# Kernel tuning notes

Measured on AMD Instinct MI355X. Metric: run time of the kernel, lower is better.

The kernel has to match this reference:

```python
import jax, jax.numpy as jnp
import numpy as np
import math

B, S, D = 2, 4096, 1024
H, HD = 16, 64
R = 16

def _rope(x, cos, sin):
    # x: [B, S, H, HD]; cos/sin: [S, HD//2]
    xr = x.reshape(*x.shape[:-1], HD // 2, 2)
    xe, xo = xr[..., 0], xr[..., 1]
    c = cos[None, :, None, :]
    s = sin[None, :, None, :]
    # complex multiply (xe + i*xo) * (c + i*s)
    re = xe * c - xo * s
    im = xe * s + xo * c
    return jnp.stack([re, im], axis=-1).reshape(x.shape)

def setup_inputs() -> dict:
    key = jax.random.key(0)
    ks = jax.random.split(key, 20)
    inp = {}
    inp["x"] = jax.random.normal(ks[0], (B, S, D), dtype=jnp.float32)
    pos = jnp.arange(S, dtype=jnp.float32)
    inv_freq = 1.0 / (10000.0 ** (jnp.arange(0, HD, 2, dtype=jnp.float32) / HD))
    ang = pos[:, None] * inv_freq[None, :]  # [S, HD//2]
    inp["freqs_cos"] = jnp.cos(ang)
    inp["freqs_sin"] = jnp.sin(ang)
    causal = jnp.triu(jnp.full((S, S), -1e9, dtype=jnp.float32), k=1)
    inp["mask"] = causal[None, None, :, :]
    sc = 1.0 / math.sqrt(D)
    inp["wq_w"] = jax.random.normal(ks[1], (D, D), dtype=jnp.float32) * sc
    inp["wq_b"] = jnp.zeros((D,), dtype=jnp.float32)
    inp["wk_w"] = jax.random.normal(ks[2], (D, D), dtype=jnp.float32) * sc
    inp["wv_w"] = jax.random.normal(ks[3], (D, D), dtype=jnp.float32) * sc
    inp["wo_w"] = jax.random.normal(ks[4], (D, D), dtype=jnp.float32) * sc
    inp["wo_b"] = jnp.zeros((D,), dtype=jnp.float32)
    for i, nm in enumerate(["q", "k", "v", "o"]):
        inp[f"lora_{nm}_l1"] = jax.random.normal(ks[5 + 2 * i], (R, D), dtype=jnp.float32) * sc
        inp[f"lora_{nm}_l2"] = jax.random.normal(ks[6 + 2 * i], (D, R), dtype=jnp.float32) * 0.01
    return inp

def reference(x, freqs_cos, freqs_sin, mask, wq_w, wq_b, wk_w, wv_w, wo_w, wo_b,
              lora_q_l1, lora_q_l2, lora_k_l1, lora_k_l2,
              lora_v_l1, lora_v_l2, lora_o_l1, lora_o_l2):
    # QKV projections + LoRA deltas (torch Linear: y = x @ W.T + b, W is [out, in])
    xq = x @ wq_w.T + wq_b + (x @ lora_q_l1.T) @ lora_q_l2.T
    xk = x @ wk_w.T + (x @ lora_k_l1.T) @ lora_k_l2.T
    xv = x @ wv_w.T + (x @ lora_v_l1.T) @ lora_v_l2.T
    xq = xq.reshape(B, S, H, HD)
    xk = xk.reshape(B, S, H, HD)
    xv = xv.reshape(B, S, H, HD)
    xq = _rope(xq, freqs_cos, freqs_sin)
    xk = _rope(xk, freqs_cos, freqs_sin)
    # attention (training path: keys/values = current xk/xv, causal mask additive)
    scores = jnp.einsum('bqhd,bkhd->bhqk', xq, xk) / math.sqrt(HD)
    scores = scores + mask
    probs = jax.nn.softmax(scores.astype(jnp.float32), axis=-1).astype(xq.dtype)
    out = jnp.einsum('bhqk,bkhd->bqhd', probs, xv).reshape(B, S, D)
    return out @ wo_w.T + wo_b + (out @ lora_o_l1.T) @ lora_o_l2.T
```

## Files before the change

### kernel.cpp

```cpp
#include <hip/hip_runtime.h>
#include <hip/hip_bf16.h>
#include <stdint.h>

#define S_DIM 4096
#define D_DIM 1024
#define KAUG  1088
#define M_ROWS 8192

typedef short bf16x8 __attribute__((ext_vector_type(8)));
typedef float f32x4  __attribute__((ext_vector_type(4)));

__device__ __forceinline__ f32x4 mfma16(bf16x8 a, bf16x8 b, f32x4 c) {
  return __builtin_amdgcn_mfma_f32_16x16x32_bf16(a, b, c, 0, 0, 0);
}
__device__ __forceinline__ short f2bs(float f) {
  __hip_bfloat16 h = __float2bfloat16(f);
  return *reinterpret_cast<short*>(&h);
}
__device__ __forceinline__ short f2bs_fast(float f) {
  unsigned u = __builtin_bit_cast(unsigned, f) + 0x8000u;
  return (short)(u >> 16);
}
__device__ __forceinline__ unsigned pk2bf(float a, float b) {
  unsigned ua = __builtin_bit_cast(unsigned, a) + 0x8000u;
  unsigned ub = __builtin_bit_cast(unsigned, b) + 0x8000u;
  return __builtin_amdgcn_perm(ub, ua, 0x07060302);
}
__device__ __forceinline__ float bs2f(short s) {
  __hip_bfloat16 h;
  *reinterpret_cast<short*>(&h) = s;
  return __bfloat162float(h);
}
__device__ __forceinline__ float fexp2(float x) {
  return __builtin_amdgcn_exp2f(x);
}
__device__ __forceinline__ void gload16(const void* g, void* l) {
  __builtin_amdgcn_global_load_lds(
      (const __attribute__((address_space(1))) unsigned int*)g,
      (__attribute__((address_space(3))) unsigned int*)l, 16, 0, 0);
}

__global__ void prep_k(const float* __restrict__ x,
                       const float* __restrict__ wq, const float* __restrict__ wk,
                       const float* __restrict__ wv, const float* __restrict__ wo,
                       const float* __restrict__ wqb,
                       const float* __restrict__ lq1, const float* __restrict__ lq2,
                       const float* __restrict__ lk1, const float* __restrict__ lk2,
                       const float* __restrict__ lv1, const float* __restrict__ lv2,
                       const float* __restrict__ lo1, const float* __restrict__ lo2,
                       const float* __restrict__ cf, const float* __restrict__ sf,
                       short* __restrict__ xaug, short* __restrict__ wqkv,
                       short* __restrict__ woaug, short* __restrict__ l1cat,
                       float* __restrict__ biasc, float* __restrict__ cs2)
{
  unsigned i = blockIdx.x * 256u + threadIdx.x;
  if (i < 8388608u) {
    unsigned m = i >> 10, k = i & 1023u;
    xaug[(size_t)m * KAUG + k] = f2bs(x[i]);
    return;
  }
  i -= 8388608u;
  if (i < 3342336u) {
    unsigned n = i / 1088u, k = i - n * 1088u;
    float v;
    if (k < 1024u) {
      v = (n < 1024u) ? wq[n * 1024u + k]
        : (n < 2048u) ? wk[(n - 1024u) * 1024u + k]
                      : wv[(n - 2048u) * 1024u + k];
    } else {
      unsigned r = k - 1024u, blk = r >> 4, which = n >> 10;
      if (blk == which) {
        const float* l2 = which == 0 ? lq2 : which == 1 ? lk2 : lv2;
        v = l2[(n & 1023u) * 16u + (r & 15u)];
      } else v = 0.f;
    }
    wqkv[i] = f2bs(v);
    return;
  }
  i -= 3342336u;
  if (i < 1114112u) {
    unsigned n = i / 1088u, k = i - n * 1088u;
    float v = (k < 1024u) ? wo[n * 1024u + k]
            : (k < 1040u) ? lo2[n * 16u + (k - 1024u)] : 0.f;
    woaug[i] = f2bs(v);
    return;
  }
  i -= 1114112u;
  if (i < 65536u) {
    unsigned r = i >> 10, k = i & 1023u;
    const float* src = r < 16u ? lq1 : r < 32u ? lk1 : r < 48u ? lv1 : lo1;
    l1cat[i] = f2bs(src[(r & 15u) * 1024u + k]);
    return;
  }
  i -= 65536u;
  if (i < 3072u) {
    biasc[i] = (i < 1024u) ? wqb[i] : 0.f;
    return;
  }
  i -= 3072u;
  if (i < 131072u) {
    cs2[2u * i]     = cf[i];
    cs2[2u * i + 1] = sf[i];
  }
}

template<int MODE>
__global__ __launch_bounds__(256) void gemm_bt(
    const short* __restrict__ A, int lda,
    const short* __restrict__ B, int ldb,
    int N, int K,
    const float* __restrict__ bias,
    void* __restrict__ Cout, int ldc, int colofs,
    short* __restrict__ qo, short* __restrict__ ko, short* __restrict__ vo,
    const float* __restrict__ cs2)
{
  __shared__ short As[128 * 32];
  __shared__ short Bs[128 * 32];
  const int tid = threadIdx.x;
  const int w = tid >> 6, lane = tid & 63;
  const int q4 = lane >> 4, c = lane & 15;
  const int mh = w >> 1, nh = w & 1;
  const int mt = blockIdx.y, nt = blockIdx.x;

  const int rl = lane >> 2;
  const int kc = (lane & 3) * 8;

  const short* Ag0 = A + (size_t)(mt * 128 + w * 32 + rl) * lda + kc;
  const short* Ag1 = Ag0 + (size_t)16 * lda;
  int rb0 = nt * 128 + w * 32 + rl;      if (rb0 > N - 1) rb0 = N - 1;
  int rb1 = nt * 128 + w * 32 + 16 + rl; if (rb1 > N - 1) rb1 = N - 1;
  const short* Bg0 = B + (size_t)rb0 * ldb + kc;
  const short* Bg1 = B + (size_t)rb1 * ldb + kc;
  short* as0 = &As[(w * 32) * 32];
  short* as1 = &As[(w * 32 + 16) * 32];
  short* bs0 = &Bs[(w * 32) * 32];
  short* bs1 = &Bs[(w * 32 + 16) * 32];

  f32x4 acc[4][4];
#pragma unroll
  for (int ms = 0; ms < 4; ++ms)
#pragma unroll
    for (int ns = 0; ns < 4; ++ns) acc[ms][ns] = (f32x4){0.f, 0.f, 0.f, 0.f};

  const int nkt = K >> 5;
  for (int kt = 0; kt < nkt; ++kt) {
    __syncthreads();
    gload16(Ag0, as0);
    gload16(Ag1, as1);
    gload16(Bg0, bs0);
    gload16(Bg1, bs1);
    Ag0 += 32; Ag1 += 32; Bg0 += 32; Bg1 += 32;
    __syncthreads();
    bf16x8 af[4], bfr[4];
#pragma unroll
    for (int ms = 0; ms < 4; ++ms)
      af[ms] = *(const bf16x8*)&As[(mh * 64 + ms * 16 + c) * 32 + q4 * 8];
#pragma unroll
    for (int ns = 0; ns < 4; ++ns)
      bfr[ns] = *(const bf16x8*)&Bs[(nh * 64 + ns * 16 + c) * 32 + q4 * 8];
#pragma unroll
    for (int ms = 0; ms < 4; ++ms)
#pragma unroll
      for (int ns = 0; ns < 4; ++ns)
        acc[ms][ns] = mfma16(af[ms], bfr[ns], acc[ms][ns]);
  }

#pragma unroll
  for (int ms = 0; ms < 4; ++ms) {
#pragma unroll
    for (int ns = 0; ns < 4; ++ns) {
      const int n = nt * 128 + nh * 64 + ns * 16 + c;
      if (MODE == 0) {
        float bsv = (n < N) ? bias[n] : 0.f;
        float* Co = (float*)Cout;
#pragma unroll
        for (int r = 0; r < 4; ++r) {
          int m = mt * 128 + mh * 64 + ms * 16 + q4 * 4 + r;
          if (n < N) Co[(size_t)m * ldc + n] = acc[ms][ns][r] + bsv;
        }
      } else if (MODE == 1) {
        short* Co = (short*)Cout;
#pragma unroll
        for (int r = 0; r < 4; ++r) {
          int m = mt * 128 + mh * 64 + ms * 16 + q4 * 4 + r;
          if (n < N) Co[(size_t)m * ldc + colofs + n] = f2bs_fast(acc[ms][ns][r]);
        }
      } else {
        float bsv = bias[n];
        int which = n >> 10;
        int m0 = mt * 128 + mh * 64 + ms * 16 + q4 * 4;
        int bb = m0 >> 12, spos = m0 & 4095;
        if (which < 2) {
          int h = (n >> 6) & 15;
          int hd = n & 63;
          short* dst = which == 0 ? qo : ko;
          const float sgn = (c & 1) ? 1.f : -1.f;
          const int ihalf = hd >> 1;
#pragma unroll
          for (int r = 0; r < 4; ++r) {
            float val = acc[ms][ns][r] + bsv;
            float part = __shfl_xor(val, 1);
            float2 cs = *(const float2*)&cs2[((size_t)(spos + r) * 32 + ihalf) * 2];
            float res = val * cs.x + part * (sgn * cs.y);
            if (which == 0) res *= 0.18033688011112042f;
            dst[(size_t)((bb * 16 + h) * 4096 + spos + r) * 64 + hd] = f2bs_fast(res);
          }
        } else {
          int h = (n >> 6) & 15;
          int hd = n & 63;
          uint2 vk;
          vk.x = pk2bf(acc[ms][ns][0] + bsv, acc[ms][ns][1] + bsv);
          vk.y = pk2bf(acc[ms][ns][2] + bsv, acc[ms][ns][3] + bsv);
          *(uint2*)&vo[(((size_t)bb * 16 + h) * 64 + hd) * 4096 + spos] = vk;
        }
      }
    }
  }
}

template<int NT>
__global__ __launch_bounds__(256) void tgemm_k(
    const short* __restrict__ A, int lda,
    const short* __restrict__ B, int ldb,
    int N, int K, short* __restrict__ C, int ldc, int colofs)
{
  __shared__ short As[64 * 32];
  __shared__ short Bs[64 * 32];
  const int tid = threadIdx.x;
  const int w = tid >> 6, lane = tid & 63;
  const int q4 = lane >> 4, c = lane & 15;
  const int rl = lane >> 2, kc = (lane & 3) * 8;
  const int arow = w * 16 + rl;
  const int brow = arow <= N - 1 ? arow : N - 1;

  const short* Ag = A + (size_t)(blockIdx.x * 64 + arow) * lda + kc;
  const short* Bg = B + (size_t)brow * ldb + kc;
  short* asd = &As[(w * 16) * 32];
  short* bsd = &Bs[(w * 16) * 32];

  f32x4 acc[NT];
#pragma unroll
  for (int i = 0; i < NT; ++i) acc[i] = (f32x4){0.f, 0.f, 0.f, 0.f};

  const int nkt = K >> 5;
  for (int kt = 0; kt < nkt; ++kt) {
    __syncthreads();
    gload16(Ag, asd);
    gload16(Bg, bsd);
    Ag += 32; Bg += 32;
    __syncthreads();
    bf16x8 af = *(const bf16x8*)&As[(w * 16 + c) * 32 + q4 * 8];
#pragma unroll
    for (int nsi = 0; nsi < NT; ++nsi) {
      bf16x8 bf = *(const bf16x8*)&Bs[(nsi * 16 + c) * 32 + q4 * 8];
      acc[nsi] = mfma16(af, bf, acc[nsi]);
    }
  }
#pragma unroll
  for (int nsi = 0; nsi < NT; ++nsi) {
#pragma unroll
    for (int r = 0; r < 4; ++r) {
      int m = blockIdx.x * 64 + w * 16 + q4 * 4 + r;
      int n = nsi * 16 + c;
      if (n < N) C[(size_t)m * ldc + colofs + n] = f2bs_fast(acc[nsi][r]);
    }
  }
}

__global__ __launch_bounds__(256, 2) void flash_k(
    const short* __restrict__ Qb, const short* __restrict__ Kb,
    const short* __restrict__ Vt, short* __restrict__ Oaug)
{
  __shared__ short lds[24576];
  short* const PL = &lds[16384];

  const int id = (int)blockIdx.y * 16 + (int)blockIdx.x;
  const int g = id & 7, j = id >> 3;
  const int bh = g * 4 + (j >> 4);
  const int bx = j & 15;

  const int tid = threadIdx.x;
  const int w = tid >> 6, lane = tid & 63;
  const int q4 = lane >> 4, c = lane & 15;

  const short* Kg = Kb + (size_t)bh * 4096 * 64;
  const short* Vg = Vt + (size_t)bh * 64 * 4096;

  const int l8 = lane >> 3, l7 = lane & 7;
  const int sw = (l7 ^ l8) * 8;
  const int G0 = w * 2, G1 = w * 2 + 1;
  const int koff0 = (G0 * 8 + l8) * 64 + sw;
  const int koff1 = (G1 * 8 + l8) * 64 + sw;
  const int voff0 = (G0 * 8 + l8) * 4096 + sw;
  const int voff1 = (G1 * 8 + l8) * 4096 + sw;
  const int qg = w * 4;
  const int qoff0 = ((qg + 0) * 8 + l8) * 64 + sw;
  const int qoff1 = ((qg + 1) * 8 + l8) * 64 + sw;
  const int qoff2 = ((qg + 2) * 8 + l8) * 64 + sw;
  const int qoff3 = ((qg + 3) * 8 + l8) * 64 + sw;

  const int c7 = c & 7;
  const int chA0 = ((q4) ^ c7) * 8;
  const int chA1 = ((4 + q4) ^ c7) * 8;
  const int rowc = c * 64;
  const int rowq = (w * 16 + c) * 64;
  const int pw_base = (w * 16 + c) * 64 + (q4 & 1) * 4;
  const int pw_g = q4 >> 1;

  const int b = bh >> 4, h = bh & 15;

  for (int half = 0; half < 2; ++half) {
    const int qt = half == 0 ? 31 - bx : bx;
    const short* Qg = Qb + ((size_t)bh * 4096 + qt * 128) * 64;

    gload16(Qg + qoff0, &lds[16384 + (qg + 0) * 512]);
    gload16(Qg + qoff1, &lds[16384 + (qg + 1) * 512]);
    gload16(Qg + qoff2, &lds[16384 + (qg + 2) * 512]);
    gload16(Qg + qoff3, &lds[16384 + (qg + 3) * 512]);
    gload16(Kg + koff0, &lds[G0 * 512]);
    gload16(Kg + koff1, &lds[G1 * 512]);
    gload16(Vg + voff0, &lds[8192 + G0 * 512]);
    gload16(Vg + voff1, &lds[8192 + G1 * 512]);
    __syncthreads();

    bf16x8 qa0 = *(const bf16x8*)(PL + rowq + chA0);
    bf16x8 qa1 = *(const bf16x8*)(PL + rowq + chA1);
    bf16x8 qb0 = *(const bf16x8*)(PL + 4096 + rowq + chA0);
    bf16x8 qb1 = *(const bf16x8*)(PL + 4096 + rowq + chA1);

    f32x4 oa[4], ob[4];
#pragma unroll
    for (int i = 0; i < 4; ++i) {
      oa[i] = (f32x4){0.f, 0.f, 0.f, 0.f};
      ob[i] = (f32x4){0.f, 0.f, 0.f, 0.f};
    }
    float la = 0.f, lb = 0.f;

    const int last = 2 * qt + 1;
    for (int kt = 0; kt <= last; ++kt) {
      const int cur = (kt & 1) * 4096;
      const short* Kc = &lds[cur];
      const short* Vc = &lds[8192 + cur];
      if (kt < last) {
        const int nxt = ((kt + 1) & 1) * 4096;
        const short* ks = Kg + (size_t)(kt + 1) * 4096;
        const short* vs = Vg + (size_t)(kt + 1) * 64;
        gload16(ks + koff0, &lds[nxt + G0 * 512]);
        gload16(ks + koff1, &lds[nxt + G1 * 512]);
        gload16(vs + voff0, &lds[8192 + nxt + G0 * 512]);
        gload16(vs + voff1, &lds[8192 + nxt + G1 * 512]);
      }
      const bool doA = (kt <= 2 * qt);

      f32x4 sa[4], sb[4];
#pragma unroll
      for (int ns = 0; ns < 4; ++ns) {
        bf16x8 kf0 = *(const bf16x8*)(Kc + ns * 1024 + rowc + chA0);
        bf16x8 kf1 = *(const bf16x8*)(Kc + ns * 1024 + rowc + chA1);
        sa[ns] = mfma16(kf0, qa0, (f32x4){0.f, 0.f, 0.f, 0.f});
        sa[ns] = mfma16(kf1, qa1, sa[ns]);
        sb[ns] = mfma16(kf0, qb0, (f32x4){0.f, 0.f, 0.f, 0.f});
        sb[ns] = mfma16(kf1, qb1, sb[ns]);
      }
      if (kt == 2 * qt) {
#pragma unroll
        for (int ns = 0; ns < 4; ++ns)
#pragma unroll
          for (int r = 0; r < 4; ++r)
            if (ns * 16 + q4 * 4 + r > w * 16 + c) sa[ns][r] = -1e30f;
      }
      if (kt == last) {
#pragma unroll
        for (int ns = 0; ns < 4; ++ns)
#pragma unroll
          for (int r = 0; r < 4; ++r)
            if (ns * 16 + q4 * 4 + r > w * 16 + c) sb[ns][r] = -1e30f;
      }

      bf16x8 pfa0, pfa1;
      if (doA) {
        float ps[4][4];
#pragma unroll
        for (int ns = 0; ns < 4; ++ns)
#pragma unroll
          for (int r = 0; r < 4; ++r) ps[ns][r] = fexp2(sa[ns][r]);
        float s0 = (ps[0][0] + ps[0][1]) + (ps[0][2] + ps[0][3]);
        float s1 = (ps[1][0] + ps[1][1]) + (ps[1][2] + ps[1][3]);
        float s2 = (ps[2][0] + ps[2][1]) + (ps[2][2] + ps[2][3]);
        float s3 = (ps[3][0] + ps[3][1]) + (ps[3][2] + ps[3][3]);
        float sum = (s0 + s1) + (s2 + s3);
        sum += __shfl_xor(sum, 16);
        sum += __shfl_xor(sum, 32);
        la += sum;
#pragma unroll
        for (int ns = 0; ns < 4; ++ns) {
          uint2 pk;
          pk.x = pk2bf(ps[ns][0], ps[ns][1]);
          pk.y = pk2bf(ps[ns][2], ps[ns][3]);
          *(uint2*)(PL + pw_base + (((ns * 2 + pw_g) ^ c7) * 8)) = pk;
        }
        pfa0 = *(const bf16x8*)(PL + rowq + chA0);
        pfa1 = *(const bf16x8*)(PL + rowq + chA1);
      }
      {
        float ps[4][4];
#pragma unroll
        for (int ns = 0; ns < 4; ++ns)
#pragma unroll
          for (int r = 0; r < 4; ++r) ps[ns][r] = fexp2(sb[ns][r]);
        float s0 = (ps[0][0] + ps[0][1]) + (ps[0][2] + ps[0][3]);
        float s1 = (ps[1][0] + ps[1][1]) + (ps[1][2] + ps[1][3]);
        float s2 = (ps[2][0] + ps[2][1]) + (ps[2][2] + ps[2][3]);
        float s3 = (ps[3][0] + ps[3][1]) + (ps[3][2] + ps[3][3]);
        float sum = (s0 + s1) + (s2 + s3);
        sum += __shfl_xor(sum, 16);
        sum += __shfl_xor(sum, 32);
        lb += sum;
#pragma unroll
        for (int ns = 0; ns < 4; ++ns) {
          uint2 pk;
          pk.x = pk2bf(ps[ns][0], ps[ns][1]);
          pk.y = pk2bf(ps[ns][2], ps[ns][3]);
          *(uint2*)(PL + 4096 + pw_base + (((ns * 2 + pw_g) ^ c7) * 8)) = pk;
        }
      }
      bf16x8 pfb0 = *(const bf16x8*)(PL + 4096 + rowq + chA0);
      bf16x8 pfb1 = *(const bf16x8*)(PL + 4096 + rowq + chA1);

#pragma unroll
      for (int nc = 0; nc < 4; ++nc) {
        bf16x8 vf0 = *(const bf16x8*)(Vc + nc * 1024 + rowc + chA0);
        bf16x8 vf1 = *(const bf16x8*)(Vc + nc * 1024 + rowc + chA1);
        if (doA) {
          oa[nc] = mfma16(vf0, pfa0, oa[nc]);
          oa[nc] = mfma16(vf1, pfa1, oa[nc]);
        }
        ob[nc] = mfma16(vf0, pfb0, ob[nc]);
        ob[nc] = mfma16(vf1, pfb1, ob[nc]);
      }
      __syncthreads();
    }

    float lia = 1.f / la, lib = 1.f / lb;
#pragma unroll
    for (int nc = 0; nc < 4; ++nc) {
      uint2 ok;
      ok.x = pk2bf(oa[nc][0] * lia, oa[nc][1] * lia);
      ok.y = pk2bf(oa[nc][2] * lia, oa[nc][3] * lia);
      *(uint2*)(PL + pw_base + (((nc * 2 + pw_g) ^ c7) * 8)) = ok;
      uint2 ok2;
      ok2.x = pk2bf(ob[nc][0] * lib, ob[nc][1] * lib);
      ok2.y = pk2bf(ob[nc][2] * lib, ob[nc][3] * lib);
      *(uint2*)(PL + 4096 + pw_base + (((nc * 2 + pw_g) ^ c7) * 8)) = ok2;
    }
    __syncthreads();
#pragma unroll
    for (int i2 = 0; i2 < 4; ++i2) {
      int ch = tid + i2 * 256;
      int r = ch >> 3, g2 = ch & 7;
      size_t row = (size_t)b * 4096 + qt * 128 + r;
      *(int4*)&Oaug[row * KAUG + h * 64 + g2 * 8] =
          *(const int4*)(PL + r * 64 + ((g2 ^ (r & 7)) * 8));
    }
    __syncthreads();
  }
}

extern "C" void kernel_launch(void* const* d_in, const int* in_sizes, int n_in,
                              void* d_out, int out_size, void* d_ws, size_t ws_size,
                              hipStream_t stream) {
  const float* x   = (const float*)d_in[0];
  const float* fc  = (const float*)d_in[1];
  const float* fs  = (const float*)d_in[2];
  const float* wq  = (const float*)d_in[4];
  const float* wqb = (const float*)d_in[5];
  const float* wk  = (const float*)d_in[6];
  const float* wv  = (const float*)d_in[7];
  const float* wo  = (const float*)d_in[8];
  const float* wob = (const float*)d_in[9];
  const float* lq1 = (const float*)d_in[10];
  const float* lq2 = (const float*)d_in[11];
  const float* lk1 = (const float*)d_in[12];
  const float* lk2 = (const float*)d_in[13];
  const float* lv1 = (const float*)d_in[14];
  const float* lv2 = (const float*)d_in[15];
  const float* lo1 = (const float*)d_in[16];
  const float* lo2 = (const float*)d_in[17];

  char* ws = (char*)d_ws;
  const size_t OFF_XAUG  = 0;
  const size_t OFF_XOAUG = 17825792;
  const size_t OFF_WQKV  = 35651584;
  const size_t OFF_WOAUG = 42336256;
  const size_t OFF_L1CAT = 44564480;
  const size_t OFF_BIASC = 44695552;
  const size_t OFF_QB    = 44707840;
  const size_t OFF_KB    = 61485056;
  const size_t OFF_VT    = 78262272;
  const size_t OFF_CS    = 95039488;

  short* xaug  = (short*)(ws + OFF_XAUG);
  short* xoaug = (short*)(ws + OFF_XOAUG);
  short* wqkv  = (short*)(ws + OFF_WQKV);
  short* woaug = (short*)(ws + OFF_WOAUG);
  short* l1cat = (short*)(ws + OFF_L1CAT);
  float* biasc = (float*)(ws + OFF_BIASC);
  short* qb    = (short*)(ws + OFF_QB);
  short* kb    = (short*)(ws + OFF_KB);
  short* vt    = (short*)(ws + OFF_VT);
  float* cs2   = (float*)(ws + OFF_CS);

  prep_k<<<50956, 256, 0, stream>>>(x, wq, wk, wv, wo, wqb,
                                    lq1, lq2, lk1, lk2, lv1, lv2, lo1, lo2,
                                    fc, fs,
                                    xaug, wqkv, woaug, l1cat, biasc, cs2);
  tgemm_k<3><<<128, 256, 0, stream>>>(xaug, KAUG, l1cat, 1024, 48, 1024,
                                      xaug, KAUG, 1024);
  gemm_bt<2><<<dim3(24, 64), 256, 0, stream>>>(xaug, KAUG, wqkv, KAUG, 3072, KAUG,
                                               biasc, nullptr, 0, 0, qb, kb, vt,
                                               cs2);
  flash_k<<<dim3(16, 32), 256, 0, stream>>>(qb, kb, vt, xoaug);
  tgemm_k<1><<<128, 256, 0, stream>>>(xoaug, KAUG, l1cat + 48 * 1024, 1024,
                                      16, 1024, xoaug, KAUG, 1024);
  gemm_bt<0><<<dim3(8, 64), 256, 0, stream>>>(xoaug, KAUG, woaug, KAUG, 1024, KAUG,
                                              wob, d_out, 1024, 0,
                                              nullptr, nullptr, nullptr, nullptr);
}
```

Baseline: 404.4 us.

## Split paired causal tiles into separate blocks and shrink LDS for higher occupancy

Each flash attention block no longer processes two query tiles (a heavy and a light one, for causal load balancing). It now handles one query tile, and the grid doubles to 1024 blocks. The P staging buffer is shared between the A and B halves, which cuts LDS from 48KB to 40KB, and launch bounds are raised to 4 blocks per CU. The heaviest tiles are scheduled first. The aim is more waves in flight to hide latency, at the cost of losing the paired-tile balancing and adding extra barriers to the epilogue.

```diff
diff --git a/kernel.cpp b/kernel.cpp
--- a/kernel.cpp
+++ b/kernel.cpp
@@ -267,17 +267,17 @@
   }
 }
 
-__global__ __launch_bounds__(256, 2) void flash_k(
+__global__ __launch_bounds__(256, 4) void flash_k(
     const short* __restrict__ Qb, const short* __restrict__ Kb,
     const short* __restrict__ Vt, short* __restrict__ Oaug)
 {
-  __shared__ short lds[24576];
+  __shared__ short lds[20480];
   short* const PL = &lds[16384];
 
-  const int id = (int)blockIdx.y * 16 + (int)blockIdx.x;
+  const int id = (int)blockIdx.y * 32 + (int)blockIdx.x;
   const int g = id & 7, j = id >> 3;
-  const int bh = g * 4 + (j >> 4);
-  const int bx = j & 15;
+  const int bh = g * 4 + (j >> 5);
+  const int qt = 31 - (j & 31);
 
   const int tid = threadIdx.x;
   const int w = tid >> 6, lane = tid & 63;
@@ -285,6 +285,7 @@
 
   const short* Kg = Kb + (size_t)bh * 4096 * 64;
   const short* Vg = Vt + (size_t)bh * 64 * 4096;
+  const short* Qg = Qb + ((size_t)bh * 4096 + qt * 128) * 64;
 
   const int l8 = lane >> 3, l7 = lane & 7;
   const int sw = (l7 ^ l8) * 8;
@@ -309,160 +310,168 @@
 
   const int b = bh >> 4, h = bh & 15;
 
-  for (int half = 0; half < 2; ++half) {
-    const int qt = half == 0 ? 31 - bx : bx;
-    const short* Qg = Qb + ((size_t)bh * 4096 + qt * 128) * 64;
-
-    gload16(Qg + qoff0, &lds[16384 + (qg + 0) * 512]);
-    gload16(Qg + qoff1, &lds[16384 + (qg + 1) * 512]);
-    gload16(Qg + qoff2, &lds[16384 + (qg + 2) * 512]);
-    gload16(Qg + qoff3, &lds[16384 + (qg + 3) * 512]);
-    gload16(Kg + koff0, &lds[G0 * 512]);
-    gload16(Kg + koff1, &lds[G1 * 512]);
-    gload16(Vg + voff0, &lds[8192 + G0 * 512]);
-    gload16(Vg + voff1, &lds[8192 + G1 * 512]);
+  gload16(Qg + qoff0, &lds[(qg + 0) * 512]);
+  gload16(Qg + qoff1, &lds[(qg + 1) * 512]);
+  gload16(Qg + qoff2, &lds[(qg + 2) * 512]);
+  gload16(Qg + qoff3, &lds[(qg + 3) * 512]);
+  __syncthreads();
+  bf16x8 qa0 = *(const bf16x8*)(&lds[0] + rowq + chA0);
+  bf16x8 qa1 = *(const bf16x8*)(&lds[0] + rowq + chA1);
+  bf16x8 qb0 = *(const bf16x8*)(&lds[4096] + rowq + chA0);
+  bf16x8 qb1 = *(const bf16x8*)(&lds[4096] + rowq + chA1);
+  __syncthreads();
+  gload16(Kg + koff0, &lds[G0 * 512]);
+  gload16(Kg + koff1, &lds[G1 * 512]);
+  gload16(Vg + voff0, &lds[8192 + G0 * 512]);
+  gload16(Vg + voff1, &lds[8192 + G1 * 512]);
+  __syncthreads();
+
+  f32x4 oa[4], ob[4];
+#pragma unroll
+  for (int i = 0; i < 4; ++i) {
+    oa[i] = (f32x4){0.f, 0.f, 0.f, 0.f};
+    ob[i] = (f32x4){0.f, 0.f, 0.f, 0.f};
+  }
+  float la = 0.f, lb = 0.f;
+
+  const int last = 2 * qt + 1;
+  for (int kt = 0; kt <= last; ++kt) {
+    const int cur = (kt & 1) * 4096;
+    const short* Kc = &lds[cur];
+    const short* Vc = &lds[8192 + cur];
+    if (kt < last) {
+      const int nxt = ((kt + 1) & 1) * 4096;
+      const short* ks = Kg + (size_t)(kt + 1) * 4096;
+      const short* vs = Vg + (size_t)(kt + 1) * 64;
+      gload16(ks + koff0, &lds[nxt + G0 * 512]);
+      gload16(ks + koff1, &lds[nxt + G1 * 512]);
+      gload16(vs + voff0, &lds[8192 + nxt + G0 * 512]);
+      gload16(vs + voff1, &lds[8192 + nxt + G1 * 512]);
+    }
+    const bool doA = (kt <= 2 * qt);
+
+    f32x4 sa[4], sb[4];
+#pragma unroll
+    for (int ns = 0; ns < 4; ++ns) {
+      bf16x8 kf0 = *(const bf16x8*)(Kc + ns * 1024 + rowc + chA0);
+      bf16x8 kf1 = *(const bf16x8*)(Kc + ns * 1024 + rowc + chA1);
+      sa[ns] = mfma16(kf0, qa0, (f32x4){0.f, 0.f, 0.f, 0.f});
+      sa[ns] = mfma16(kf1, qa1, sa[ns]);
+      sb[ns] = mfma16(kf0, qb0, (f32x4){0.f, 0.f, 0.f, 0.f});
+      sb[ns] = mfma16(kf1, qb1, sb[ns]);
+    }
+    if (kt == 2 * qt) {
+#pragma unroll
+      for (int ns = 0; ns < 4; ++ns)
+#pragma unroll
+        for (int r = 0; r < 4; ++r)
+          if (ns * 16 + q4 * 4 + r > w * 16 + c) sa[ns][r] = -1e30f;
+    }
+    if (kt == last) {
+#pragma unroll
+      for (int ns = 0; ns < 4; ++ns)
+#pragma unroll
+        for (int r = 0; r < 4; ++r)
+          if (ns * 16 + q4 * 4 + r > w * 16 + c) sb[ns][r] = -1e30f;
+    }
+
+    bf16x8 pfa0, pfa1;
+    if (doA) {
+      float ps[4][4];
+#pragma unroll
+      for (int ns = 0; ns < 4; ++ns)
+#pragma unroll
+        for (int r = 0; r < 4; ++r) ps[ns][r] = fexp2(sa[ns][r]);
+      float s0 = (ps[0][0] + ps[0][1]) + (ps[0][2] + ps[0][3]);
+      float s1 = (ps[1][0] + ps[1][1]) + (ps[1][2] + ps[1][3]);
+      float s2 = (ps[2][0] + ps[2][1]) + (ps[2][2] + ps[2][3]);
+      float s3 = (ps[3][0] + ps[3][1]) + (ps[3][2] + ps[3][3]);
+      float sum = (s0 + s1) + (s2 + s3);
+      sum += __shfl_xor(sum, 16);
+      sum += __shfl_xor(sum, 32);
+      la += sum;
+#pragma unroll
+      for (int ns = 0; ns < 4; ++ns) {
+        uint2 pk;
+        pk.x = pk2bf(ps[ns][0], ps[ns][1]);
+        pk.y = pk2bf(ps[ns][2], ps[ns][3]);
+        *(uint2*)(PL + pw_base + (((ns * 2 + pw_g) ^ c7) * 8)) = pk;
+      }
+      pfa0 = *(const bf16x8*)(PL + rowq + chA0);
+      pfa1 = *(const bf16x8*)(PL + rowq + chA1);
+    }
+    {
+      float ps[4][4];
+#pragma unroll
+      for (int ns = 0; ns < 4; ++ns)
+#pragma unroll
+        for (int r = 0; r < 4; ++r) ps[ns][r] = fexp2(sb[ns][r]);
+      float s0 = (ps[0][0] + ps[0][1]) + (ps[0][2] + ps[0][3]);
+      float s1 = (ps[1][0] + ps[1][1]) + (ps[1][2] + ps[1][3]);
+      float s2 = (ps[2][0] + ps[2][1]) + (ps[2][2] + ps[2][3]);
+      float s3 = (ps[3][0] + ps[3][1]) + (ps[3][2] + ps[3][3]);
+      float sum = (s0 + s1) + (s2 + s3);
+      sum += __shfl_xor(sum, 16);
+      sum += __shfl_xor(sum, 32);
+      lb += sum;
+#pragma unroll
+      for (int ns = 0; ns < 4; ++ns) {
+        uint2 pk;
+        pk.x = pk2bf(ps[ns][0], ps[ns][1]);
+        pk.y = pk2bf(ps[ns][2], ps[ns][3]);
+        *(uint2*)(PL + pw_base + (((ns * 2 + pw_g) ^ c7) * 8)) = pk;
+      }
+    }
+    bf16x8 pfb0 = *(const bf16x8*)(PL + rowq + chA0);
+    bf16x8 pfb1 = *(const bf16x8*)(PL + rowq + chA1);
+
+#pragma unroll
+    for (int nc = 0; nc < 4; ++nc) {
+      bf16x8 vf0 = *(const bf16x8*)(Vc + nc * 1024 + rowc + chA0);
+      bf16x8 vf1 = *(const bf16x8*)(Vc + nc * 1024 + rowc + chA1);
+      if (doA) {
+        oa[nc] = mfma16(vf0, pfa0, oa[nc]);
+        oa[nc] = mfma16(vf1, pfa1, oa[nc]);
+      }
+      ob[nc] = mfma16(vf0, pfb0, ob[nc]);
+      ob[nc] = mfma16(vf1, pfb1, ob[nc]);
+    }
     __syncthreads();
-
-    bf16x8 qa0 = *(const bf16x8*)(PL + rowq + chA0);
-    bf16x8 qa1 = *(const bf16x8*)(PL + rowq + chA1);
-    bf16x8 qb0 = *(const bf16x8*)(PL + 4096 + rowq + chA0);
-    bf16x8 qb1 = *(const bf16x8*)(PL + 4096 + rowq + chA1);
-
-    f32x4 oa[4], ob[4];
-#pragma unroll
-    for (int i = 0; i < 4; ++i) {
-      oa[i] = (f32x4){0.f, 0.f, 0.f, 0.f};
-      ob[i] = (f32x4){0.f, 0.f, 0.f, 0.f};
-    }
-    float la = 0.f, lb = 0.f;
-
-    const int last = 2 * qt + 1;
-    for (int kt = 0; kt <= last; ++kt) {
-      const int cur = (kt & 1) * 4096;
-      const short* Kc = &lds[cur];
-      const short* Vc = &lds[8192 + cur];
-      if (kt < last) {
-        const int nxt = ((kt + 1) & 1) * 4096;
-        const short* ks = Kg + (size_t)(kt + 1) * 4096;
-        const short* vs = Vg + (size_t)(kt + 1) * 64;
-        gload16(ks + koff0, &lds[nxt + G0 * 512]);
-        gload16(ks + koff1, &lds[nxt + G1 * 512]);
-        gload16(vs + voff0, &lds[8192 + nxt + G0 * 512]);
-        gload16(vs + voff1, &lds[8192 + nxt + G1 * 512]);
-      }
-      const bool doA = (kt <= 2 * qt);
-
-      f32x4 sa[4], sb[4];
-#pragma unroll
-      for (int ns = 0; ns < 4; ++ns) {
-        bf16x8 kf0 = *(const bf16x8*)(Kc + ns * 1024 + rowc + chA0);
-        bf16x8 kf1 = *(const bf16x8*)(Kc + ns * 1024 + rowc + chA1);
-        sa[ns] = mfma16(kf0, qa0, (f32x4){0.f, 0.f, 0.f, 0.f});
-        sa[ns] = mfma16(kf1, qa1, sa[ns]);
-        sb[ns] = mfma16(kf0, qb0, (f32x4){0.f, 0.f, 0.f, 0.f});
-        sb[ns] = mfma16(kf1, qb1, sb[ns]);
-      }
-      if (kt == 2 * qt) {
-#pragma unroll
-        for (int ns = 0; ns < 4; ++ns)
-#pragma unroll
-          for (int r = 0; r < 4; ++r)
-            if (ns * 16 + q4 * 4 + r > w * 16 + c) sa[ns][r] = -1e30f;
-      }
-      if (kt == last) {
-#pragma unroll
-        for (int ns = 0; ns < 4; ++ns)
-#pragma unroll
-          for (int r = 0; r < 4; ++r)
-            if (ns * 16 + q4 * 4 + r > w * 16 + c) sb[ns][r] = -1e30f;
-      }
-
-      bf16x8 pfa0, pfa1;
-      if (doA) {
-        float ps[4][4];
-#pragma unroll
-        for (int ns = 0; ns < 4; ++ns)
-#pragma unroll
-          for (int r = 0; r < 4; ++r) ps[ns][r] = fexp2(sa[ns][r]);
-        float s0 = (ps[0][0] + ps[0][1]) + (ps[0][2] + ps[0][3]);
-        float s1 = (ps[1][0] + ps[1][1]) + (ps[1][2] + ps[1][3]);
-        float s2 = (ps[2][0] + ps[2][1]) + (ps[2][2] + ps[2][3]);
-        float s3 = (ps[3][0] + ps[3][1]) + (ps[3][2] + ps[3][3]);
-        float sum = (s0 + s1) + (s2 + s3);
-        sum += __shfl_xor(sum, 16);
-        sum += __shfl_xor(sum, 32);
-        la += sum;
-#pragma unroll
-        for (int ns = 0; ns < 4; ++ns) {
-          uint2 pk;
-          pk.x = pk2bf(ps[ns][0], ps[ns][1]);
-          pk.y = pk2bf(ps[ns][2], ps[ns][3]);
-          *(uint2*)(PL + pw_base + (((ns * 2 + pw_g) ^ c7) * 8)) = pk;
-        }
-        pfa0 = *(const bf16x8*)(PL + rowq + chA0);
-        pfa1 = *(const bf16x8*)(PL + rowq + chA1);
-      }
-      {
-        float ps[4][4];
-#pragma unroll
-        for (int ns = 0; ns < 4; ++ns)
-#pragma unroll
-          for (int r = 0; r < 4; ++r) ps[ns][r] = fexp2(sb[ns][r]);
-        float s0 = (ps[0][0] + ps[0][1]) + (ps[0][2] + ps[0][3]);
-        float s1 = (ps[1][0] + ps[1][1]) + (ps[1][2] + ps[1][3]);
-        float s2 = (ps[2][0] + ps[2][1]) + (ps[2][2] + ps[2][3]);
-        float s3 = (ps[3][0] + ps[3][1]) + (ps[3][2] + ps[3][3]);
-        float sum = (s0 + s1) + (s2 + s3);
-        sum += __shfl_xor(sum, 16);
-        sum += __shfl_xor(sum, 32);
-        lb += sum;
-#pragma unroll
-        for (int ns = 0; ns < 4; ++ns) {
-          uint2 pk;
-          pk.x = pk2bf(ps[ns][0], ps[ns][1]);
-          pk.y = pk2bf(ps[ns][2], ps[ns][3]);
-          *(uint2*)(PL + 4096 + pw_base + (((ns * 2 + pw_g) ^ c7) * 8)) = pk;
-        }
-      }
-      bf16x8 pfb0 = *(const bf16x8*)(PL + 4096 + rowq + chA0);
-      bf16x8 pfb1 = *(const bf16x8*)(PL + 4096 + rowq + chA1);
-
-#pragma unroll
-      for (int nc = 0; nc < 4; ++nc) {
-        bf16x8 vf0 = *(const bf16x8*)(Vc + nc * 1024 + rowc + chA0);
-        bf16x8 vf1 = *(const bf16x8*)(Vc + nc * 1024 + rowc + chA1);
-        if (doA) {
-          oa[nc] = mfma16(vf0, pfa0, oa[nc]);
-          oa[nc] = mfma16(vf1, pfa1, oa[nc]);
-        }
-        ob[nc] = mfma16(vf0, pfb0, ob[nc]);
-        ob[nc] = mfma16(vf1, pfb1, ob[nc]);
-      }
-      __syncthreads();
-    }
-
-    float lia = 1.f / la, lib = 1.f / lb;
-#pragma unroll
-    for (int nc = 0; nc < 4; ++nc) {
-      uint2 ok;
-      ok.x = pk2bf(oa[nc][0] * lia, oa[nc][1] * lia);
-      ok.y = pk2bf(oa[nc][2] * lia, oa[nc][3] * lia);
-      *(uint2*)(PL + pw_base + (((nc * 2 + pw_g) ^ c7) * 8)) = ok;
-      uint2 ok2;
-      ok2.x = pk2bf(ob[nc][0] * lib, ob[nc][1] * lib);
-      ok2.y = pk2bf(ob[nc][2] * lib, ob[nc][3] * lib);
-      *(uint2*)(PL + 4096 + pw_base + (((nc * 2 + pw_g) ^ c7) * 8)) = ok2;
-    }
-    __syncthreads();
-#pragma unroll
-    for (int i2 = 0; i2 < 4; ++i2) {
-      int ch = tid + i2 * 256;
-      int r = ch >> 3, g2 = ch & 7;
-      size_t row = (size_t)b * 4096 + qt * 128 + r;
-      *(int4*)&Oaug[row * KAUG + h * 64 + g2 * 8] =
-          *(const int4*)(PL + r * 64 + ((g2 ^ (r & 7)) * 8));
-    }
-    __syncthreads();
+  }
+
+  float lia = 1.f / la, lib = 1.f / lb;
+#pragma unroll
+  for (int nc = 0; nc < 4; ++nc) {
+    uint2 ok;
+    ok.x = pk2bf(oa[nc][0] * lia, oa[nc][1] * lia);
+    ok.y = pk2bf(oa[nc][2] * lia, oa[nc][3] * lia);
+    *(uint2*)(PL + pw_base + (((nc * 2 + pw_g) ^ c7) * 8)) = ok;
+  }
+  __syncthreads();
+#pragma unroll
+  for (int i2 = 0; i2 < 2; ++i2) {
+    int ch = tid + i2 * 256;
+    int r = ch >> 3, g2 = ch & 7;
+    size_t row = (size_t)b * 4096 + qt * 128 + r;
+    *(int4*)&Oaug[row * KAUG + h * 64 + g2 * 8] =
+        *(const int4*)(PL + r * 64 + ((g2 ^ (r & 7)) * 8));
+  }
+  __syncthreads();
+#pragma unroll
+  for (int nc = 0; nc < 4; ++nc) {
+    uint2 ok;
+    ok.x = pk2bf(ob[nc][0] * lib, ob[nc][1] * lib);
+    ok.y = pk2bf(ob[nc][2] * lib, ob[nc][3] * lib);
+    *(uint2*)(PL + pw_base + (((nc * 2 + pw_g) ^ c7) * 8)) = ok;
+  }
+  __syncthreads();
+#pragma unroll
+  for (int i2 = 0; i2 < 2; ++i2) {
+    int ch = tid + i2 * 256;
+    int r = ch >> 3, g2 = ch & 7;
+    size_t row = (size_t)b * 4096 + qt * 128 + 64 + r;
+    *(int4*)&Oaug[row * KAUG + h * 64 + g2 * 8] =
+        *(const int4*)(PL + r * 64 + ((g2 ^ (r & 7)) * 8));
   }
 }
 
@@ -519,7 +528,7 @@
   gemm_bt<2><<<dim3(24, 64), 256, 0, stream>>>(xaug, KAUG, wqkv, KAUG, 3072, KAUG,
                                                biasc, nullptr, 0, 0, qb, kb, vt,
                                                cs2);
-  flash_k<<<dim3(16, 32), 256, 0, stream>>>(qb, kb, vt, xoaug);
+  flash_k<<<dim3(32, 32), 256, 0, stream>>>(qb, kb, vt, xoaug);
   tgemm_k<1><<<128, 256, 0, stream>>>(xoaug, KAUG, l1cat + 48 * 1024, 1024,
                                       16, 1024, xoaug, KAUG, 1024);
   gemm_bt<0><<<dim3(8, 64), 256, 0, stream>>>(xoaug, KAUG, woaug, KAUG, 1024, KAUG,
```

Result: slower. 470.4 us (+16.3%).
